# Kernel optimization log

Hardware: AMD Instinct MI355X
Metric: run time of the kernel (lower is better)

The kernel has to match this reference:

```python
import jax, jax.numpy as jnp
import numpy as np

B, T, D = 4, 4096, 1024
N, L = 2048, 768
H = 16
EPS = 1e-5

def layernorm(x, g, b):
    mu = jnp.mean(x, axis=-1, keepdims=True)
    var = jnp.mean((x - mu) ** 2, axis=-1, keepdims=True)
    return (x - mu) * jax.lax.rsqrt(var + EPS) * g + b

def setup_inputs() -> dict:
    key = jax.random.key(0)
    ks = jax.random.split(key, 8)
    s_d = 1.0 / np.sqrt(D)
    s_l = 1.0 / np.sqrt(L)
    return {
        "x1": jax.random.normal(ks[0], (B, T, D), jnp.float32),
        "x2": jax.random.normal(ks[1], (B, N, L), jnp.float32),
        "Wq": jax.random.normal(ks[2], (D, D), jnp.float32) * s_d,
        "bq": jnp.zeros((D,), jnp.float32),
        "Wk": jax.random.normal(ks[3], (L, D), jnp.float32) * s_l,
        "bk": jnp.zeros((D,), jnp.float32),
        "Wv": jax.random.normal(ks[4], (L, D), jnp.float32) * s_l,
        "bv": jnp.zeros((D,), jnp.float32),
        "Wh": jax.random.normal(ks[5], (D, D), jnp.float32) * s_d,
        "bh": jnp.zeros((D,), jnp.float32),
        "g1": jnp.ones((D,), jnp.float32),
        "b1": jnp.zeros((D,), jnp.float32),
        "g2": jnp.ones((L,), jnp.float32),
        "b2": jnp.zeros((L,), jnp.float32),
    }

def reference(x1, x2, Wq, bq, Wk, bk, Wv, bv, Wh, bh, g1, b1, g2, b2):
    nx1 = layernorm(x1, g1, b1)
    nx2 = layernorm(x2, g2, b2)
    q = (nx1 @ Wq + bq).reshape(B, T, H, D // H)
    k = (nx2 @ Wk + bk).reshape(B, N, H, D // H)
    v = (nx2 @ Wv + bv).reshape(B, N, H, D // H)
    q = jax.nn.softmax(q, axis=-1)
    k = jax.nn.softmax(k, axis=-1)
    # dropout p=0 -> identity
    attn = jnp.einsum('bnhd,bnhl->bhdl', k, v)          # [B,H,dh,dh]
    y = jnp.einsum('bthd,bhdl->bthl', q, attn).reshape(B, T, D)
    return x1 @ Wh + bh + y
```

## Files before the change

kernel.cpp:

```cpp
#include <hip/hip_runtime.h>


#define DEV __device__ __forceinline__

typedef unsigned short bf16_t;
typedef __attribute__((ext_vector_type(8))) __bf16 bf16x8;
typedef __attribute__((ext_vector_type(8))) unsigned short ushort8;
typedef __attribute__((ext_vector_type(4))) float f32x4;

DEV unsigned short f2bf(float f) {
  unsigned int u = __float_as_uint(f);
  unsigned int r = 0x7FFFu + ((u >> 16) & 1u);
  return (unsigned short)((u + r) >> 16);
}
DEV float bf2f(unsigned short u) { return __uint_as_float(((unsigned int)u) << 16); }

DEV void gld16(const void* g, void* l) {
  __builtin_amdgcn_global_load_lds((__attribute__((address_space(1))) void*)g,
                                   (__attribute__((address_space(3))) void*)l, 16, 0, 0);
}

__global__ __launch_bounds__(256) void wprep_kernel(
    const float* __restrict__ Wq, const float* __restrict__ Wk,
    const float* __restrict__ Wv, const float* __restrict__ Wh,
    bf16_t* __restrict__ Wqf, bf16_t* __restrict__ Wkf,
    bf16_t* __restrict__ Wvf, bf16_t* __restrict__ Whf) {
  int t = blockIdx.x;
  const float* src; bf16_t* dst; int KB;
  if (t < 1024)      { src = Wq; dst = Wqf; KB = 32; }
  else if (t < 1792) { src = Wk; dst = Wkf; KB = 24; t -= 1024; }
  else if (t < 2560) { src = Wv; dst = Wvf; KB = 24; t -= 1792; }
  else               { src = Wh; dst = Whf; KB = 32; t -= 2560; }
  int tk = t >> 5, tn = t & 31;
  __shared__ float tile[32][33];
  int tx = threadIdx.x & 31, ty = threadIdx.x >> 5;
#pragma unroll
  for (int i = 0; i < 4; ++i) {
    int r = ty + i * 8;
    tile[r][tx] = src[(size_t)(tk * 32 + r) * 1024 + tn * 32 + tx];
  }
  __syncthreads();
  int tid = threadIdx.x;
  if (tid < 128) {
    int rt = tid >> 6, p = (tid >> 4) & 3, ri = tid & 15;
    ushort8 v;
#pragma unroll
    for (int ko = 0; ko < 8; ++ko)
      v[ko] = f2bf(tile[p * 8 + ko][rt * 16 + ri]);
    size_t off = ((size_t)(tn * 2 + rt) * KB + tk) * 512 + p * 128 + ri * 8;
    *(ushort8*)&dst[off] = v;
  }
}

__global__ __launch_bounds__(256) void ln1_kernel(
    const float* __restrict__ x1, const float* __restrict__ g1, const float* __restrict__ b1,
    bf16_t* __restrict__ nx1f, bf16_t* __restrict__ x1f) {
  __shared__ bf16_t stash[16 * 1032];
  __shared__ float murs[16][2];
  int rt = blockIdx.x, tid = threadIdx.x;
  {
    int rowl = tid >> 4, ci = tid & 15;
    size_t base = ((size_t)rt * 16 + rowl) * 1024;
    float s = 0.f, s2 = 0.f;
#pragma unroll
    for (int j = 0; j < 16; ++j) {
      int k0 = ci * 4 + j * 64;
      float4 f = *(const float4*)&x1[base + k0];
      s += f.x + f.y + f.z + f.w;
      s2 += f.x * f.x + f.y * f.y + f.z * f.z + f.w * f.w;
      ushort4 u;
      u.x = f2bf(f.x); u.y = f2bf(f.y); u.z = f2bf(f.z); u.w = f2bf(f.w);
      *(ushort4*)&stash[rowl * 1032 + k0] = u;
    }
#pragma unroll
    for (int off = 1; off < 16; off <<= 1) {
      s  += __shfl_xor(s, off);
      s2 += __shfl_xor(s2, off);
    }
    if (ci == 0) {
      float mu = s * (1.0f / 1024.0f);
      float var = s2 * (1.0f / 1024.0f) - mu * mu;
      murs[rowl][0] = mu;
      murs[rowl][1] = rsqrtf(var + 1e-5f);
    }
  }
  __syncthreads();
  {
    int ri = tid & 15, pg = tid >> 4;
    float mu = murs[ri][0], rs = murs[ri][1];
#pragma unroll
    for (int t = 0; t < 8; ++t) {
      int P = pg * 8 + t;
      ushort8 raw = *(const ushort8*)&stash[ri * 1032 + P * 8];
      float4 ga = *(const float4*)&g1[P * 8], gb = *(const float4*)&g1[P * 8 + 4];
      float4 ba = *(const float4*)&b1[P * 8], bb = *(const float4*)&b1[P * 8 + 4];
      float gv[8] = {ga.x, ga.y, ga.z, ga.w, gb.x, gb.y, gb.z, gb.w};
      float bv[8] = {ba.x, ba.y, ba.z, ba.w, bb.x, bb.y, bb.z, bb.w};
      ushort8 nv;
#pragma unroll
      for (int ko = 0; ko < 8; ++ko)
        nv[ko] = f2bf((bf2f(raw[ko]) - mu) * rs * gv[ko] + bv[ko]);
      size_t off = ((size_t)rt * 32 + (P >> 2)) * 512 + (P & 3) * 128 + ri * 8;
      *(ushort8*)&nx1f[off] = nv;
      *(ushort8*)&x1f[off] = raw;
    }
  }
}

__global__ __launch_bounds__(256) void ln2_kernel(
    const float* __restrict__ x2, const float* __restrict__ g2, const float* __restrict__ b2,
    bf16_t* __restrict__ nx2f) {
  __shared__ bf16_t stash[16 * 776];
  __shared__ float murs[16][2];
  int rt = blockIdx.x, tid = threadIdx.x;
  {
    int rowl = tid >> 4, ci = tid & 15;
    size_t base = ((size_t)rt * 16 + rowl) * 768;
    float s = 0.f, s2 = 0.f;
#pragma unroll
    for (int j = 0; j < 12; ++j) {
      int k0 = ci * 4 + j * 64;
      float4 f = *(const float4*)&x2[base + k0];
      s += f.x + f.y + f.z + f.w;
      s2 += f.x * f.x + f.y * f.y + f.z * f.z + f.w * f.w;
      ushort4 u;
      u.x = f2bf(f.x); u.y = f2bf(f.y); u.z = f2bf(f.z); u.w = f2bf(f.w);
      *(ushort4*)&stash[rowl * 776 + k0] = u;
    }
#pragma unroll
    for (int off = 1; off < 16; off <<= 1) {
      s  += __shfl_xor(s, off);
      s2 += __shfl_xor(s2, off);
    }
    if (ci == 0) {
      float mu = s * (1.0f / 768.0f);
      float var = s2 * (1.0f / 768.0f) - mu * mu;
      murs[rowl][0] = mu;
      murs[rowl][1] = rsqrtf(var + 1e-5f);
    }
  }
  __syncthreads();
  {
    int ri = tid & 15, pg = tid >> 4;
    float mu = murs[ri][0], rs = murs[ri][1];
#pragma unroll
    for (int t = 0; t < 6; ++t) {
      int P = pg * 6 + t;
      ushort8 raw = *(const ushort8*)&stash[ri * 776 + P * 8];
      float4 ga = *(const float4*)&g2[P * 8], gb = *(const float4*)&g2[P * 8 + 4];
      float4 ba = *(const float4*)&b2[P * 8], bb = *(const float4*)&b2[P * 8 + 4];
      float gv[8] = {ga.x, ga.y, ga.z, ga.w, gb.x, gb.y, gb.z, gb.w};
      float bv[8] = {ba.x, ba.y, ba.z, ba.w, bb.x, bb.y, bb.z, bb.w};
      ushort8 nv;
#pragma unroll
      for (int ko = 0; ko < 8; ++ko)
        nv[ko] = f2bf((bf2f(raw[ko]) - mu) * rs * gv[ko] + bv[ko]);
      size_t off = ((size_t)rt * 24 + (P >> 2)) * 512 + (P & 3) * 128 + ri * 8;
      *(ushort8*)&nx2f[off] = nv;
    }
  }
}

__global__ __launch_bounds__(256, 2) void gemm_qkv_kernel(
    const bf16_t* __restrict__ nx1f, const bf16_t* __restrict__ Wqf,
    const float* __restrict__ bq, bf16_t* __restrict__ qout,
    const bf16_t* __restrict__ nx2f, const bf16_t* __restrict__ Wkf,
    const float* __restrict__ bk, bf16_t* __restrict__ kout,
    const bf16_t* __restrict__ Wvf, const float* __restrict__ bv,
    bf16_t* __restrict__ vout) {
  __shared__ bf16_t Bs[2 * 16 * 512];
  int id = blockIdx.x;
  const bf16_t *A, *BT; const float* bias; bf16_t* out;
  int nk, bm, bn, do_softmax;
  if (id < 512) {
    A = nx1f; BT = Wqf; bias = bq; out = qout; nk = 32;
    bm = id & 127; bn = id >> 7; do_softmax = 1;
  } else if (id < 768) {
    id -= 512; A = nx2f; BT = Wkf; bias = bk; out = kout; nk = 24;
    bm = id & 63; bn = id >> 6; do_softmax = 1;
  } else {
    id -= 768; A = nx2f; BT = Wvf; bias = bv; out = vout; nk = 24;
    bm = id & 63; bn = id >> 6; do_softmax = 0;
  }
  int tid = threadIdx.x, lane = tid & 63, wid = tid >> 6;
  int wm = wid & 1, wn = wid >> 1;

  const bf16_t* ap[4];
#pragma unroll
  for (int mi = 0; mi < 4; ++mi)
    ap[mi] = A + ((size_t)(bm * 8 + wm * 4 + mi) * nk) * 512 + lane * 8;
  const bf16_t* sp[4];
#pragma unroll
  for (int i = 0; i < 4; ++i)
    sp[i] = BT + ((size_t)(bn * 16 + wid * 4 + i) * nk) * 512 + lane * 8;

  f32x4 acc[4][8];
#pragma unroll
  for (int i = 0; i < 4; ++i)
#pragma unroll
    for (int j = 0; j < 8; ++j) acc[i][j] = {0.f, 0.f, 0.f, 0.f};

  bf16x8 acur[4], anxt[4];
#pragma unroll
  for (int i = 0; i < 4; ++i)
    gld16(sp[i], (void*)&Bs[(wid * 4 + i) * 512 + lane * 8]);
#pragma unroll
  for (int mi = 0; mi < 4; ++mi) acur[mi] = *(const bf16x8*)ap[mi];

  for (int kt = 0; kt < nk; ++kt) {
    int cb = kt & 1;
    if (kt + 1 < nk) {
      int nb = cb ^ 1;
#pragma unroll
      for (int i = 0; i < 4; ++i)
        gld16(sp[i] + (kt + 1) * 512, (void*)&Bs[nb * 8192 + (wid * 4 + i) * 512 + lane * 8]);
#pragma unroll
      for (int mi = 0; mi < 4; ++mi) anxt[mi] = *(const bf16x8*)(ap[mi] + (kt + 1) * 512);
      asm volatile("s_waitcnt vmcnt(8)\n\ts_barrier" ::: "memory");
    } else {
      asm volatile("s_waitcnt vmcnt(0)\n\ts_barrier" ::: "memory");
    }
    bf16x8 bfr[8];
#pragma unroll
    for (int ni = 0; ni < 8; ++ni)
      bfr[ni] = *(const bf16x8*)&Bs[cb * 8192 + (wn * 8 + ni) * 512 + lane * 8];
#pragma unroll
    for (int mi = 0; mi < 4; ++mi)
#pragma unroll
      for (int ni = 0; ni < 8; ++ni)
        acc[mi][ni] = __builtin_amdgcn_mfma_f32_16x16x32_bf16(acur[mi], bfr[ni], acc[mi][ni], 0, 0, 0);
    asm volatile("s_waitcnt lgkmcnt(0)\n\ts_barrier" ::: "memory");
#pragma unroll
    for (int mi = 0; mi < 4; ++mi) acur[mi] = anxt[mi];
  }

  int colg0 = bn * 256 + wn * 128;
  float bvv[8];
#pragma unroll
  for (int ni = 0; ni < 8; ++ni) bvv[ni] = bias[colg0 + ni * 16 + (lane & 15)];
#pragma unroll
  for (int mi = 0; mi < 4; ++mi) {
#pragma unroll
    for (int r = 0; r < 4; ++r) {
      int row = bm * 128 + wm * 64 + mi * 16 + (lane >> 4) * 4 + r;
      float vx[8];
#pragma unroll
      for (int ni = 0; ni < 8; ++ni) vx[ni] = acc[mi][ni][r] + bvv[ni];
      if (do_softmax) {
#pragma unroll
        for (int g = 0; g < 2; ++g) {
          float ssum = 0.f;
#pragma unroll
          for (int j = 0; j < 4; ++j) { vx[g * 4 + j] = __expf(vx[g * 4 + j]); ssum += vx[g * 4 + j]; }
#pragma unroll
          for (int off = 1; off < 16; off <<= 1) ssum += __shfl_xor(ssum, off);
          float inv = 1.0f / ssum;
#pragma unroll
          for (int j = 0; j < 4; ++j) vx[g * 4 + j] *= inv;
        }
      }
#pragma unroll
      for (int ni = 0; ni < 8; ++ni)
        out[(size_t)row * 1024 + colg0 + ni * 16 + (lane & 15)] = f2bf(vx[ni]);
    }
  }
}

__global__ __launch_bounds__(256) void attn_partial_kernel(
    const bf16_t* __restrict__ kq, const bf16_t* __restrict__ vq,
    float* __restrict__ part) {
  int bh = blockIdx.x >> 3, c = blockIdx.x & 7;
  int b = bh >> 4, h = bh & 15;
  int tid = threadIdx.x;
  int td = tid & 15, tl = tid >> 4;
  __shared__ float ks[32][64];
  __shared__ float vs[32][64];
  float acc[4][4];
#pragma unroll
  for (int i = 0; i < 4; ++i)
#pragma unroll
    for (int j = 0; j < 4; ++j) acc[i][j] = 0.f;
  for (int s = 0; s < 8; ++s) {
    __syncthreads();
    int nr = tid >> 3, col = (tid & 7) * 8;
    int n = c * 256 + s * 32 + nr;
    size_t goff = ((size_t)(b * 2048 + n)) * 1024 + h * 64 + col;
    ushort8 lk = *(const ushort8*)&kq[goff];
    ushort8 lv = *(const ushort8*)&vq[goff];
#pragma unroll
    for (int j = 0; j < 8; ++j) {
      ks[nr][col + j] = bf2f(lk[j]);
      vs[nr][col + j] = bf2f(lv[j]);
    }
    __syncthreads();
#pragma unroll
    for (int nn = 0; nn < 32; ++nn) {
      float4 kv = *(const float4*)&ks[nn][td * 4];
      float4 vv = *(const float4*)&vs[nn][tl * 4];
      float ka[4] = {kv.x, kv.y, kv.z, kv.w};
      float va[4] = {vv.x, vv.y, vv.z, vv.w};
#pragma unroll
      for (int i = 0; i < 4; ++i)
#pragma unroll
        for (int j = 0; j < 4; ++j) acc[i][j] += ka[i] * va[j];
    }
  }
#pragma unroll
  for (int i = 0; i < 4; ++i)
#pragma unroll
    for (int j = 0; j < 4; ++j) {
      int d = td * 4 + i, l = tl * 4 + j;
      part[(((size_t)bh * 8 + c) * 64 + d) * 64 + l] = acc[i][j];
    }
}

__global__ __launch_bounds__(256) void attn_finalize_kernel(
    const float* __restrict__ part, bf16_t* __restrict__ attnT) {
  int bh = blockIdx.x, tid = threadIdx.x;
  for (int t = tid; t < 4096; t += 256) {
    int d = t >> 6, l = t & 63;
    float s = 0.f;
#pragma unroll
    for (int c = 0; c < 8; ++c)
      s += part[(((size_t)bh * 8 + c) * 64 + d) * 64 + l];
    attnT[((size_t)bh * 64 + l) * 64 + d] = f2bf(s);
  }
}

__global__ __launch_bounds__(256, 2) void gemm_final_kernel(
    const bf16_t* __restrict__ x1f, const bf16_t* __restrict__ Whf,
    const float* __restrict__ bias, const bf16_t* __restrict__ qb,
    const bf16_t* __restrict__ attnT, float* __restrict__ out) {
  __shared__ bf16_t Bs[2 * 16 * 512];
  const int nk = 32;
  int tid = threadIdx.x;
  int bm = blockIdx.x, bn = blockIdx.y;
  int lane = tid & 63, wid = tid >> 6;
  int wm = wid & 1, wn = wid >> 1;
  int b = bm >> 5;
  int klane = (lane >> 4) * 8;

  const bf16_t* ap[4];
#pragma unroll
  for (int mi = 0; mi < 4; ++mi)
    ap[mi] = x1f + ((size_t)(bm * 8 + wm * 4 + mi) * nk) * 512 + lane * 8;
  const bf16_t* sp[4];
#pragma unroll
  for (int i = 0; i < 4; ++i)
    sp[i] = Whf + ((size_t)(bn * 16 + wid * 4 + i) * nk) * 512 + lane * 8;

  f32x4 acc[4][8];
#pragma unroll
  for (int i = 0; i < 4; ++i)
#pragma unroll
    for (int j = 0; j < 8; ++j) acc[i][j] = {0.f, 0.f, 0.f, 0.f};

  bf16x8 acur[4], anxt[4];
#pragma unroll
  for (int i = 0; i < 4; ++i)
    gld16(sp[i], (void*)&Bs[(wid * 4 + i) * 512 + lane * 8]);
#pragma unroll
  for (int mi = 0; mi < 4; ++mi) acur[mi] = *(const bf16x8*)ap[mi];

  for (int kt = 0; kt < nk; ++kt) {
    int cb = kt & 1;
    if (kt + 1 < nk) {
      int nb = cb ^ 1;
#pragma unroll
      for (int i = 0; i < 4; ++i)
        gld16(sp[i] + (kt + 1) * 512, (void*)&Bs[nb * 8192 + (wid * 4 + i) * 512 + lane * 8]);
#pragma unroll
      for (int mi = 0; mi < 4; ++mi) anxt[mi] = *(const bf16x8*)(ap[mi] + (kt + 1) * 512);
      asm volatile("s_waitcnt vmcnt(8)\n\ts_barrier" ::: "memory");
    } else {
      asm volatile("s_waitcnt vmcnt(0)\n\ts_barrier" ::: "memory");
    }
    bf16x8 bfr[8];
#pragma unroll
    for (int ni = 0; ni < 8; ++ni)
      bfr[ni] = *(const bf16x8*)&Bs[cb * 8192 + (wn * 8 + ni) * 512 + lane * 8];
#pragma unroll
    for (int mi = 0; mi < 4; ++mi)
#pragma unroll
      for (int ni = 0; ni < 8; ++ni)
        acc[mi][ni] = __builtin_amdgcn_mfma_f32_16x16x32_bf16(acur[mi], bfr[ni], acc[mi][ni], 0, 0, 0);
    asm volatile("s_waitcnt lgkmcnt(0)\n\ts_barrier" ::: "memory");
#pragma unroll
    for (int mi = 0; mi < 4; ++mi) acur[mi] = anxt[mi];
  }

  {
    int h0 = bn * 4 + wn * 2;
#pragma unroll
    for (int k2 = 0; k2 < 2; ++k2) {
      bf16x8 aq[2][4], bt[8];
#pragma unroll
      for (int g = 0; g < 2; ++g)
#pragma unroll
        for (int mi = 0; mi < 4; ++mi)
          aq[g][mi] = *(const bf16x8*)(qb
              + (size_t)(bm * 128 + wm * 64 + mi * 16 + (lane & 15)) * 1024
              + (h0 + g) * 64 + k2 * 32 + klane);
#pragma unroll
      for (int ni = 0; ni < 8; ++ni)
        bt[ni] = *(const bf16x8*)(attnT
            + ((size_t)(b * 16 + h0 + (ni >> 2)) * 64 + (ni & 3) * 16 + (lane & 15)) * 64
            + k2 * 32 + klane);
#pragma unroll
      for (int mi = 0; mi < 4; ++mi)
#pragma unroll
        for (int ni = 0; ni < 8; ++ni)
          acc[mi][ni] = __builtin_amdgcn_mfma_f32_16x16x32_bf16(aq[ni >> 2][mi], bt[ni], acc[mi][ni], 0, 0, 0);
    }
  }

  int colg0 = bn * 256 + wn * 128;
  float bvv[8];
#pragma unroll
  for (int ni = 0; ni < 8; ++ni) bvv[ni] = bias[colg0 + ni * 16 + (lane & 15)];
#pragma unroll
  for (int mi = 0; mi < 4; ++mi)
#pragma unroll
    for (int r = 0; r < 4; ++r) {
      int row = bm * 128 + wm * 64 + mi * 16 + (lane >> 4) * 4 + r;
#pragma unroll
      for (int ni = 0; ni < 8; ++ni)
        out[(size_t)row * 1024 + colg0 + ni * 16 + (lane & 15)] = acc[mi][ni][r] + bvv[ni];
    }
}

extern "C" void kernel_launch(void* const* d_in, const int* in_sizes, int n_in,
                              void* d_out, int out_size, void* d_ws, size_t ws_size,
                              hipStream_t stream) {
  const float* x1 = (const float*)d_in[0];
  const float* x2 = (const float*)d_in[1];
  const float* Wq = (const float*)d_in[2];
  const float* bq = (const float*)d_in[3];
  const float* Wk = (const float*)d_in[4];
  const float* bk = (const float*)d_in[5];
  const float* Wv = (const float*)d_in[6];
  const float* bv = (const float*)d_in[7];
  const float* Wh = (const float*)d_in[8];
  const float* bh = (const float*)d_in[9];
  const float* g1 = (const float*)d_in[10];
  const float* b1 = (const float*)d_in[11];
  const float* g2 = (const float*)d_in[12];
  const float* b2 = (const float*)d_in[13];
  float* out = (float*)d_out;

  char* w = (char*)d_ws;
  bf16_t* nx1f = (bf16_t*)w; w += (size_t)16384 * 1024 * 2;
  bf16_t* x1f  = (bf16_t*)w; w += (size_t)16384 * 1024 * 2;
  bf16_t* nx2f = (bf16_t*)w; w += (size_t)8192 * 768 * 2;
  bf16_t* Wqf  = (bf16_t*)w; w += (size_t)1024 * 1024 * 2;
  bf16_t* Wkf  = (bf16_t*)w; w += (size_t)1024 * 768 * 2;
  bf16_t* Wvf  = (bf16_t*)w; w += (size_t)1024 * 768 * 2;
  bf16_t* Whf  = (bf16_t*)w; w += (size_t)1024 * 1024 * 2;
  bf16_t* qb   = (bf16_t*)w; w += (size_t)16384 * 1024 * 2;
  bf16_t* kbuf = (bf16_t*)w; w += (size_t)8192 * 1024 * 2;
  bf16_t* vbuf = (bf16_t*)w; w += (size_t)8192 * 1024 * 2;
  float*  part = (float*)w;  w += (size_t)64 * 8 * 64 * 64 * 4;
  bf16_t* attnT = (bf16_t*)w; w += (size_t)64 * 64 * 64 * 2;

  wprep_kernel<<<dim3(3584), dim3(256), 0, stream>>>(Wq, Wk, Wv, Wh, Wqf, Wkf, Wvf, Whf);
  ln1_kernel<<<dim3(1024), dim3(256), 0, stream>>>(x1, g1, b1, nx1f, x1f);
  ln2_kernel<<<dim3(512), dim3(256), 0, stream>>>(x2, g2, b2, nx2f);
  gemm_qkv_kernel<<<dim3(1024), dim3(256), 0, stream>>>(
      nx1f, Wqf, bq, qb, nx2f, Wkf, bk, kbuf, Wvf, bv, vbuf);
  attn_partial_kernel<<<dim3(512), dim3(256), 0, stream>>>(kbuf, vbuf, part);
  attn_finalize_kernel<<<dim3(64), dim3(256), 0, stream>>>(part, attnT);
  gemm_final_kernel<<<dim3(128, 4), dim3(256), 0, stream>>>(x1f, Whf, bh, qb, attnT, out);
}
```

Baseline: 316.6 us.

## Deepen GEMM k-loop pipeline to triple buffering with prefetch distance two

Replaces the double-buffered K loop in the QKV and final GEMM kernels with a shared templated loop that keeps three LDS stages and three A-register sets. Loads run two k-steps ahead, with vmcnt waits adjusted to match, so more memory latency is hidden behind MFMA work. In exchange the LDS footprint grows from 32KB to 48KB per block and register pressure rises, which could lower occupancy at launch_bounds(256,2).

```diff
diff --git a/kernel.cpp b/kernel.cpp
--- a/kernel.cpp
+++ b/kernel.cpp
@@ -18,6 +18,65 @@
 DEV void gld16(const void* g, void* l) {
   __builtin_amdgcn_global_load_lds((__attribute__((address_space(1))) void*)g,
                                    (__attribute__((address_space(3))) void*)l, 16, 0, 0);
+}
+
+template <int NK>
+DEV void kloop3(const bf16_t* const ap[4], const bf16_t* const sp[4],
+                bf16_t* Bs, int lane, int wid, int wn, f32x4 acc[4][8]) {
+  bf16x8 a0[4], a1[4], a2[4];
+#pragma unroll
+  for (int i = 0; i < 4; ++i)
+    gld16(sp[i], (void*)&Bs[(wid * 4 + i) * 512 + lane * 8]);
+#pragma unroll
+  for (int mi = 0; mi < 4; ++mi) a0[mi] = *(const bf16x8*)ap[mi];
+#pragma unroll
+  for (int i = 0; i < 4; ++i)
+    gld16(sp[i] + 512, (void*)&Bs[8192 + (wid * 4 + i) * 512 + lane * 8]);
+#pragma unroll
+  for (int mi = 0; mi < 4; ++mi) a1[mi] = *(const bf16x8*)(ap[mi] + 512);
+
+#define KSTEP(ktv, PH, ACUR, AFILL, ISSUE, VMSTR)                                      \
+  do {                                                                                 \
+    if (ISSUE) {                                                                       \
+      _Pragma("unroll")                                                                \
+      for (int i = 0; i < 4; ++i)                                                      \
+        gld16(sp[i] + ((ktv) + 2) * 512,                                               \
+              (void*)&Bs[(((PH) + 2) % 3) * 8192 + (wid * 4 + i) * 512 + lane * 8]);   \
+      _Pragma("unroll")                                                                \
+      for (int mi = 0; mi < 4; ++mi)                                                   \
+        AFILL[mi] = *(const bf16x8*)(ap[mi] + ((ktv) + 2) * 512);                      \
+    }                                                                                  \
+    asm volatile("s_waitcnt " VMSTR "\n\ts_barrier" ::: "memory");                     \
+    bf16x8 bfr[8];                                                                     \
+    _Pragma("unroll")                                                                  \
+    for (int ni = 0; ni < 8; ++ni)                                                     \
+      bfr[ni] = *(const bf16x8*)&Bs[(PH) * 8192 + (wn * 8 + ni) * 512 + lane * 8];     \
+    _Pragma("unroll")                                                                  \
+    for (int mi = 0; mi < 4; ++mi)                                                     \
+      _Pragma("unroll")                                                                \
+      for (int ni = 0; ni < 8; ++ni)                                                   \
+        acc[mi][ni] =                                                                  \
+            __builtin_amdgcn_mfma_f32_16x16x32_bf16(ACUR[mi], bfr[ni], acc[mi][ni],    \
+                                                    0, 0, 0);                          \
+    asm volatile("s_waitcnt lgkmcnt(0)\n\ts_barrier" ::: "memory");                    \
+  } while (0)
+
+  constexpr int TFULL = (NK - (NK % 3 == 0 ? 3 : 2)) / 3;
+  for (int kb = 0; kb < TFULL; ++kb) {
+    int kt = kb * 3;
+    KSTEP(kt,     0, a0, a2, true, "vmcnt(16)");
+    KSTEP(kt + 1, 1, a1, a0, true, "vmcnt(16)");
+    KSTEP(kt + 2, 2, a2, a1, true, "vmcnt(16)");
+  }
+  if constexpr (NK % 3 == 0) {
+    KSTEP(NK - 3, 0, a0, a2, true,  "vmcnt(16)");
+    KSTEP(NK - 2, 1, a1, a0, false, "vmcnt(8)");
+    KSTEP(NK - 1, 2, a2, a1, false, "vmcnt(0)");
+  } else {
+    KSTEP(NK - 2, 0, a0, a2, false, "vmcnt(8)");
+    KSTEP(NK - 1, 1, a1, a0, false, "vmcnt(0)");
+  }
+#undef KSTEP
 }
 
 __global__ __launch_bounds__(256) void wprep_kernel(
@@ -168,7 +227,7 @@
     const float* __restrict__ bk, bf16_t* __restrict__ kout,
     const bf16_t* __restrict__ Wvf, const float* __restrict__ bv,
     bf16_t* __restrict__ vout) {
-  __shared__ bf16_t Bs[2 * 16 * 512];
+  __shared__ bf16_t Bs[3 * 16 * 512];
   int id = blockIdx.x;
   const bf16_t *A, *BT; const float* bias; bf16_t* out;
   int nk, bm, bn, do_softmax;
@@ -200,39 +259,8 @@
 #pragma unroll
     for (int j = 0; j < 8; ++j) acc[i][j] = {0.f, 0.f, 0.f, 0.f};
 
-  bf16x8 acur[4], anxt[4];
-#pragma unroll
-  for (int i = 0; i < 4; ++i)
-    gld16(sp[i], (void*)&Bs[(wid * 4 + i) * 512 + lane * 8]);
-#pragma unroll
-  for (int mi = 0; mi < 4; ++mi) acur[mi] = *(const bf16x8*)ap[mi];
-
-  for (int kt = 0; kt < nk; ++kt) {
-    int cb = kt & 1;
-    if (kt + 1 < nk) {
-      int nb = cb ^ 1;
-#pragma unroll
-      for (int i = 0; i < 4; ++i)
-        gld16(sp[i] + (kt + 1) * 512, (void*)&Bs[nb * 8192 + (wid * 4 + i) * 512 + lane * 8]);
-#pragma unroll
-      for (int mi = 0; mi < 4; ++mi) anxt[mi] = *(const bf16x8*)(ap[mi] + (kt + 1) * 512);
-      asm volatile("s_waitcnt vmcnt(8)\n\ts_barrier" ::: "memory");
-    } else {
-      asm volatile("s_waitcnt vmcnt(0)\n\ts_barrier" ::: "memory");
-    }
-    bf16x8 bfr[8];
-#pragma unroll
-    for (int ni = 0; ni < 8; ++ni)
-      bfr[ni] = *(const bf16x8*)&Bs[cb * 8192 + (wn * 8 + ni) * 512 + lane * 8];
-#pragma unroll
-    for (int mi = 0; mi < 4; ++mi)
-#pragma unroll
-      for (int ni = 0; ni < 8; ++ni)
-        acc[mi][ni] = __builtin_amdgcn_mfma_f32_16x16x32_bf16(acur[mi], bfr[ni], acc[mi][ni], 0, 0, 0);
-    asm volatile("s_waitcnt lgkmcnt(0)\n\ts_barrier" ::: "memory");
-#pragma unroll
-    for (int mi = 0; mi < 4; ++mi) acur[mi] = anxt[mi];
-  }
+  if (nk == 32) kloop3<32>(ap, sp, Bs, lane, wid, wn, acc);
+  else          kloop3<24>(ap, sp, Bs, lane, wid, wn, acc);
 
   int colg0 = bn * 256 + wn * 128;
   float bvv[8];
@@ -331,7 +359,7 @@
     const bf16_t* __restrict__ x1f, const bf16_t* __restrict__ Whf,
     const float* __restrict__ bias, const bf16_t* __restrict__ qb,
     const bf16_t* __restrict__ attnT, float* __restrict__ out) {
-  __shared__ bf16_t Bs[2 * 16 * 512];
+  __shared__ bf16_t Bs[3 * 16 * 512];
   const int nk = 32;
   int tid = threadIdx.x;
   int bm = blockIdx.x, bn = blockIdx.y;
@@ -355,39 +383,7 @@
 #pragma unroll
     for (int j = 0; j < 8; ++j) acc[i][j] = {0.f, 0.f, 0.f, 0.f};
 
-  bf16x8 acur[4], anxt[4];
-#pragma unroll
-  for (int i = 0; i < 4; ++i)
-    gld16(sp[i], (void*)&Bs[(wid * 4 + i) * 512 + lane * 8]);
-#pragma unroll
-  for (int mi = 0; mi < 4; ++mi) acur[mi] = *(const bf16x8*)ap[mi];
-
-  for (int kt = 0; kt < nk; ++kt) {
-    int cb = kt & 1;
-    if (kt + 1 < nk) {
-      int nb = cb ^ 1;
-#pragma unroll
-      for (int i = 0; i < 4; ++i)
-        gld16(sp[i] + (kt + 1) * 512, (void*)&Bs[nb * 8192 + (wid * 4 + i) * 512 + lane * 8]);
-#pragma unroll
-      for (int mi = 0; mi < 4; ++mi) anxt[mi] = *(const bf16x8*)(ap[mi] + (kt + 1) * 512);
-      asm volatile("s_waitcnt vmcnt(8)\n\ts_barrier" ::: "memory");
-    } else {
-      asm volatile("s_waitcnt vmcnt(0)\n\ts_barrier" ::: "memory");
-    }
-    bf16x8 bfr[8];
-#pragma unroll
-    for (int ni = 0; ni < 8; ++ni)
-      bfr[ni] = *(const bf16x8*)&Bs[cb * 8192 + (wn * 8 + ni) * 512 + lane * 8];
-#pragma unroll
-    for (int mi = 0; mi < 4; ++mi)
-#pragma unroll
-      for (int ni = 0; ni < 8; ++ni)
-        acc[mi][ni] = __builtin_amdgcn_mfma_f32_16x16x32_bf16(acur[mi], bfr[ni], acc[mi][ni], 0, 0, 0);
-    asm volatile("s_waitcnt lgkmcnt(0)\n\ts_barrier" ::: "memory");
-#pragma unroll
-    for (int mi = 0; mi < 4; ++mi) acur[mi] = anxt[mi];
-  }
+  kloop3<32>(ap, sp, Bs, lane, wid, wn, acc);
 
   {
     int h0 = bn * 4 + wn * 2;
```

Measured after the change: 431.6 us. +36.3%, slower.

## Deepen GEMM B-tile pipeline to four LDS stages and drop second barrier

Applied to the files above, without the earlier changes.

Both GEMM kernels now run a shared k-loop helper that keeps four LDS buffers for the weight tiles and prefetches two k-steps ahead instead of one. The second per-iteration barrier with its lgkmcnt wait is removed, relying on the four-deep ring to stop a buffer being overwritten while another wave still reads it. The aim is to hide more global-load latency and cut synchronisation per k-step. The cost is doubled LDS per block (64 KB), which may reduce occupancy below the two blocks per CU set by the launch bounds.

```diff
diff --git a/kernel.cpp b/kernel.cpp
--- a/kernel.cpp
+++ b/kernel.cpp
@@ -18,6 +18,70 @@
 DEV void gld16(const void* g, void* l) {
   __builtin_amdgcn_global_load_lds((__attribute__((address_space(1))) void*)g,
                                    (__attribute__((address_space(3))) void*)l, 16, 0, 0);
+}
+
+DEV void kloop(int nk, const bf16_t* const ap[4], const bf16_t* const sp[4],
+               bf16_t* Bs, int lane, int wid, int wn, f32x4 acc[4][8]) {
+  bf16x8 acur[4], anxt[4];
+#pragma unroll
+  for (int i = 0; i < 4; ++i)
+    gld16(sp[i], (void*)&Bs[(wid * 4 + i) * 512 + lane * 8]);
+#pragma unroll
+  for (int mi = 0; mi < 4; ++mi) acur[mi] = *(const bf16x8*)ap[mi];
+#pragma unroll
+  for (int i = 0; i < 4; ++i)
+    gld16(sp[i] + 512, (void*)&Bs[8192 + (wid * 4 + i) * 512 + lane * 8]);
+
+  for (int kt = 0; kt < nk - 2; ++kt) {
+#pragma unroll
+    for (int mi = 0; mi < 4; ++mi)
+      anxt[mi] = *(const bf16x8*)(ap[mi] + (kt + 1) * 512);
+#pragma unroll
+    for (int i = 0; i < 4; ++i)
+      gld16(sp[i] + (kt + 2) * 512,
+            (void*)&Bs[((kt + 2) & 3) * 8192 + (wid * 4 + i) * 512 + lane * 8]);
+    asm volatile("s_waitcnt vmcnt(12)\n\ts_barrier" ::: "memory");
+    bf16x8 bfr[8];
+#pragma unroll
+    for (int ni = 0; ni < 8; ++ni)
+      bfr[ni] = *(const bf16x8*)&Bs[(kt & 3) * 8192 + (wn * 8 + ni) * 512 + lane * 8];
+#pragma unroll
+    for (int mi = 0; mi < 4; ++mi)
+#pragma unroll
+      for (int ni = 0; ni < 8; ++ni)
+        acc[mi][ni] = __builtin_amdgcn_mfma_f32_16x16x32_bf16(acur[mi], bfr[ni], acc[mi][ni], 0, 0, 0);
+#pragma unroll
+    for (int mi = 0; mi < 4; ++mi) acur[mi] = anxt[mi];
+  }
+  {
+#pragma unroll
+    for (int mi = 0; mi < 4; ++mi)
+      anxt[mi] = *(const bf16x8*)(ap[mi] + (nk - 1) * 512);
+    asm volatile("s_waitcnt vmcnt(8)\n\ts_barrier" ::: "memory");
+    bf16x8 bfr[8];
+#pragma unroll
+    for (int ni = 0; ni < 8; ++ni)
+      bfr[ni] = *(const bf16x8*)&Bs[((nk - 2) & 3) * 8192 + (wn * 8 + ni) * 512 + lane * 8];
+#pragma unroll
+    for (int mi = 0; mi < 4; ++mi)
+#pragma unroll
+      for (int ni = 0; ni < 8; ++ni)
+        acc[mi][ni] = __builtin_amdgcn_mfma_f32_16x16x32_bf16(acur[mi], bfr[ni], acc[mi][ni], 0, 0, 0);
+#pragma unroll
+    for (int mi = 0; mi < 4; ++mi) acur[mi] = anxt[mi];
+  }
+  {
+    asm volatile("s_waitcnt vmcnt(0)\n\ts_barrier" ::: "memory");
+    bf16x8 bfr[8];
+#pragma unroll
+    for (int ni = 0; ni < 8; ++ni)
+      bfr[ni] = *(const bf16x8*)&Bs[((nk - 1) & 3) * 8192 + (wn * 8 + ni) * 512 + lane * 8];
+#pragma unroll
+    for (int mi = 0; mi < 4; ++mi)
+#pragma unroll
+      for (int ni = 0; ni < 8; ++ni)
+        acc[mi][ni] = __builtin_amdgcn_mfma_f32_16x16x32_bf16(acur[mi], bfr[ni], acc[mi][ni], 0, 0, 0);
+  }
 }
 
 __global__ __launch_bounds__(256) void wprep_kernel(
@@ -168,7 +232,7 @@
     const float* __restrict__ bk, bf16_t* __restrict__ kout,
     const bf16_t* __restrict__ Wvf, const float* __restrict__ bv,
     bf16_t* __restrict__ vout) {
-  __shared__ bf16_t Bs[2 * 16 * 512];
+  __shared__ bf16_t Bs[4 * 16 * 512];
   int id = blockIdx.x;
   const bf16_t *A, *BT; const float* bias; bf16_t* out;
   int nk, bm, bn, do_softmax;
@@ -200,39 +264,7 @@
 #pragma unroll
     for (int j = 0; j < 8; ++j) acc[i][j] = {0.f, 0.f, 0.f, 0.f};
 
-  bf16x8 acur[4], anxt[4];
-#pragma unroll
-  for (int i = 0; i < 4; ++i)
-    gld16(sp[i], (void*)&Bs[(wid * 4 + i) * 512 + lane * 8]);
-#pragma unroll
-  for (int mi = 0; mi < 4; ++mi) acur[mi] = *(const bf16x8*)ap[mi];
-
-  for (int kt = 0; kt < nk; ++kt) {
-    int cb = kt & 1;
-    if (kt + 1 < nk) {
-      int nb = cb ^ 1;
-#pragma unroll
-      for (int i = 0; i < 4; ++i)
-        gld16(sp[i] + (kt + 1) * 512, (void*)&Bs[nb * 8192 + (wid * 4 + i) * 512 + lane * 8]);
-#pragma unroll
-      for (int mi = 0; mi < 4; ++mi) anxt[mi] = *(const bf16x8*)(ap[mi] + (kt + 1) * 512);
-      asm volatile("s_waitcnt vmcnt(8)\n\ts_barrier" ::: "memory");
-    } else {
-      asm volatile("s_waitcnt vmcnt(0)\n\ts_barrier" ::: "memory");
-    }
-    bf16x8 bfr[8];
-#pragma unroll
-    for (int ni = 0; ni < 8; ++ni)
-      bfr[ni] = *(const bf16x8*)&Bs[cb * 8192 + (wn * 8 + ni) * 512 + lane * 8];
-#pragma unroll
-    for (int mi = 0; mi < 4; ++mi)
-#pragma unroll
-      for (int ni = 0; ni < 8; ++ni)
-        acc[mi][ni] = __builtin_amdgcn_mfma_f32_16x16x32_bf16(acur[mi], bfr[ni], acc[mi][ni], 0, 0, 0);
-    asm volatile("s_waitcnt lgkmcnt(0)\n\ts_barrier" ::: "memory");
-#pragma unroll
-    for (int mi = 0; mi < 4; ++mi) acur[mi] = anxt[mi];
-  }
+  kloop(nk, ap, sp, Bs, lane, wid, wn, acc);
 
   int colg0 = bn * 256 + wn * 128;
   float bvv[8];
@@ -331,7 +363,7 @@
     const bf16_t* __restrict__ x1f, const bf16_t* __restrict__ Whf,
     const float* __restrict__ bias, const bf16_t* __restrict__ qb,
     const bf16_t* __restrict__ attnT, float* __restrict__ out) {
-  __shared__ bf16_t Bs[2 * 16 * 512];
+  __shared__ bf16_t Bs[4 * 16 * 512];
   const int nk = 32;
   int tid = threadIdx.x;
   int bm = blockIdx.x, bn = blockIdx.y;
@@ -355,39 +387,7 @@
 #pragma unroll
     for (int j = 0; j < 8; ++j) acc[i][j] = {0.f, 0.f, 0.f, 0.f};
 
-  bf16x8 acur[4], anxt[4];
-#pragma unroll
-  for (int i = 0; i < 4; ++i)
-    gld16(sp[i], (void*)&Bs[(wid * 4 + i) * 512 + lane * 8]);
-#pragma unroll
-  for (int mi = 0; mi < 4; ++mi) acur[mi] = *(const bf16x8*)ap[mi];
-
-  for (int kt = 0; kt < nk; ++kt) {
-    int cb = kt & 1;
-    if (kt + 1 < nk) {
-      int nb = cb ^ 1;
-#pragma unroll
-      for (int i = 0; i < 4; ++i)
-        gld16(sp[i] + (kt + 1) * 512, (void*)&Bs[nb * 8192 + (wid * 4 + i) * 512 + lane * 8]);
-#pragma unroll
-      for (int mi = 0; mi < 4; ++mi) anxt[mi] = *(const bf16x8*)(ap[mi] + (kt + 1) * 512);
-      asm volatile("s_waitcnt vmcnt(8)\n\ts_barrier" ::: "memory");
-    } else {
-      asm volatile("s_waitcnt vmcnt(0)\n\ts_barrier" ::: "memory");
-    }
-    bf16x8 bfr[8];
-#pragma unroll
-    for (int ni = 0; ni < 8; ++ni)
-      bfr[ni] = *(const bf16x8*)&Bs[cb * 8192 + (wn * 8 + ni) * 512 + lane * 8];
-#pragma unroll
-    for (int mi = 0; mi < 4; ++mi)
-#pragma unroll
-      for (int ni = 0; ni < 8; ++ni)
-        acc[mi][ni] = __builtin_amdgcn_mfma_f32_16x16x32_bf16(acur[mi], bfr[ni], acc[mi][ni], 0, 0, 0);
-    asm volatile("s_waitcnt lgkmcnt(0)\n\ts_barrier" ::: "memory");
-#pragma unroll
-    for (int mi = 0; mi < 4; ++mi) acur[mi] = anxt[mi];
-  }
+  kloop(nk, ap, sp, Bs, lane, wid, wn, acc);
 
   {
     int h0 = bn * 4 + wn * 2;
```

After: 318.3 us. Within noise of the previous version (+0.5%).

## Merge weight-prep and layernorm kernels; use MFMA for K^T V partials

Applied to the files above, without the earlier changes.

Folds the three preprocessing kernels (weight transpose/convert, LN1, LN2) into a single launch that dispatches on block index, sharing one LDS buffer. This removes two launch gaps and lets the small kernels run concurrently. It also rewrites the per-head K^T V partial reduction to stage K and V transposed in bf16 LDS and use 16x16x32 bf16 MFMA instead of scalar FP32 FMAs. The shared LDS is sized for the largest branch, which may lower occupancy for the weight blocks.

```diff
diff --git a/kernel.cpp b/kernel.cpp
--- a/kernel.cpp
+++ b/kernel.cpp
@@ -20,143 +20,149 @@
                                    (__attribute__((address_space(3))) void*)l, 16, 0, 0);
 }
 
-__global__ __launch_bounds__(256) void wprep_kernel(
+__global__ __launch_bounds__(256) void prep_kernel(
     const float* __restrict__ Wq, const float* __restrict__ Wk,
     const float* __restrict__ Wv, const float* __restrict__ Wh,
     bf16_t* __restrict__ Wqf, bf16_t* __restrict__ Wkf,
-    bf16_t* __restrict__ Wvf, bf16_t* __restrict__ Whf) {
-  int t = blockIdx.x;
-  const float* src; bf16_t* dst; int KB;
-  if (t < 1024)      { src = Wq; dst = Wqf; KB = 32; }
-  else if (t < 1792) { src = Wk; dst = Wkf; KB = 24; t -= 1024; }
-  else if (t < 2560) { src = Wv; dst = Wvf; KB = 24; t -= 1792; }
-  else               { src = Wh; dst = Whf; KB = 32; t -= 2560; }
-  int tk = t >> 5, tn = t & 31;
-  __shared__ float tile[32][33];
-  int tx = threadIdx.x & 31, ty = threadIdx.x >> 5;
-#pragma unroll
-  for (int i = 0; i < 4; ++i) {
-    int r = ty + i * 8;
-    tile[r][tx] = src[(size_t)(tk * 32 + r) * 1024 + tn * 32 + tx];
-  }
-  __syncthreads();
-  int tid = threadIdx.x;
-  if (tid < 128) {
-    int rt = tid >> 6, p = (tid >> 4) & 3, ri = tid & 15;
-    ushort8 v;
-#pragma unroll
-    for (int ko = 0; ko < 8; ++ko)
-      v[ko] = f2bf(tile[p * 8 + ko][rt * 16 + ri]);
-    size_t off = ((size_t)(tn * 2 + rt) * KB + tk) * 512 + p * 128 + ri * 8;
-    *(ushort8*)&dst[off] = v;
-  }
-}
-
-__global__ __launch_bounds__(256) void ln1_kernel(
-    const float* __restrict__ x1, const float* __restrict__ g1, const float* __restrict__ b1,
-    bf16_t* __restrict__ nx1f, bf16_t* __restrict__ x1f) {
-  __shared__ bf16_t stash[16 * 1032];
+    bf16_t* __restrict__ Wvf, bf16_t* __restrict__ Whf,
+    const float* __restrict__ x1, const float* __restrict__ g1,
+    const float* __restrict__ b1, bf16_t* __restrict__ nx1f,
+    bf16_t* __restrict__ x1f,
+    const float* __restrict__ x2, const float* __restrict__ g2,
+    const float* __restrict__ b2, bf16_t* __restrict__ nx2f) {
+  __shared__ __align__(16) char smem[16 * 1032 * 2];
   __shared__ float murs[16][2];
-  int rt = blockIdx.x, tid = threadIdx.x;
+  int blk = blockIdx.x, tid = threadIdx.x;
+
+  if (blk < 3584) {
+    int t = blk;
+    const float* src; bf16_t* dst; int KB;
+    if (t < 1024)      { src = Wq; dst = Wqf; KB = 32; }
+    else if (t < 1792) { src = Wk; dst = Wkf; KB = 24; t -= 1024; }
+    else if (t < 2560) { src = Wv; dst = Wvf; KB = 24; t -= 1792; }
+    else               { src = Wh; dst = Whf; KB = 32; t -= 2560; }
+    int tk = t >> 5, tn = t & 31;
+    float (*tile)[33] = (float(*)[33])smem;
+    int tx = tid & 31, ty = tid >> 5;
+#pragma unroll
+    for (int i = 0; i < 4; ++i) {
+      int r = ty + i * 8;
+      tile[r][tx] = src[(size_t)(tk * 32 + r) * 1024 + tn * 32 + tx];
+    }
+    __syncthreads();
+    if (tid < 128) {
+      int rt = tid >> 6, p = (tid >> 4) & 3, ri = tid & 15;
+      ushort8 v;
+#pragma unroll
+      for (int ko = 0; ko < 8; ++ko)
+        v[ko] = f2bf(tile[p * 8 + ko][rt * 16 + ri]);
+      size_t off = ((size_t)(tn * 2 + rt) * KB + tk) * 512 + p * 128 + ri * 8;
+      *(ushort8*)&dst[off] = v;
+    }
+    return;
+  }
+
+  if (blk < 4608) {
+    bf16_t* stash = (bf16_t*)smem;
+    int rt = blk - 3584;
+    {
+      int rowl = tid >> 4, ci = tid & 15;
+      size_t base = ((size_t)rt * 16 + rowl) * 1024;
+      float s = 0.f, s2 = 0.f;
+#pragma unroll
+      for (int j = 0; j < 16; ++j) {
+        int k0 = ci * 4 + j * 64;
+        float4 f = *(const float4*)&x1[base + k0];
+        s += f.x + f.y + f.z + f.w;
+        s2 += f.x * f.x + f.y * f.y + f.z * f.z + f.w * f.w;
+        ushort4 u;
+        u.x = f2bf(f.x); u.y = f2bf(f.y); u.z = f2bf(f.z); u.w = f2bf(f.w);
+        *(ushort4*)&stash[rowl * 1032 + k0] = u;
+      }
+#pragma unroll
+      for (int off = 1; off < 16; off <<= 1) {
+        s  += __shfl_xor(s, off);
+        s2 += __shfl_xor(s2, off);
+      }
+      if (ci == 0) {
+        float mu = s * (1.0f / 1024.0f);
+        float var = s2 * (1.0f / 1024.0f) - mu * mu;
+        murs[rowl][0] = mu;
+        murs[rowl][1] = rsqrtf(var + 1e-5f);
+      }
+    }
+    __syncthreads();
+    {
+      int ri = tid & 15, pg = tid >> 4;
+      float mu = murs[ri][0], rs = murs[ri][1];
+#pragma unroll
+      for (int t = 0; t < 8; ++t) {
+        int P = pg * 8 + t;
+        ushort8 raw = *(const ushort8*)&stash[ri * 1032 + P * 8];
+        float4 ga = *(const float4*)&g1[P * 8], gb = *(const float4*)&g1[P * 8 + 4];
+        float4 ba = *(const float4*)&b1[P * 8], bb = *(const float4*)&b1[P * 8 + 4];
+        float gv[8] = {ga.x, ga.y, ga.z, ga.w, gb.x, gb.y, gb.z, gb.w};
+        float bv[8] = {ba.x, ba.y, ba.z, ba.w, bb.x, bb.y, bb.z, bb.w};
+        ushort8 nv;
+#pragma unroll
+        for (int ko = 0; ko < 8; ++ko)
+          nv[ko] = f2bf((bf2f(raw[ko]) - mu) * rs * gv[ko] + bv[ko]);
+        size_t off = ((size_t)rt * 32 + (P >> 2)) * 512 + (P & 3) * 128 + ri * 8;
+        *(ushort8*)&nx1f[off] = nv;
+        *(ushort8*)&x1f[off] = raw;
+      }
+    }
+    return;
+  }
+
   {
-    int rowl = tid >> 4, ci = tid & 15;
-    size_t base = ((size_t)rt * 16 + rowl) * 1024;
-    float s = 0.f, s2 = 0.f;
-#pragma unroll
-    for (int j = 0; j < 16; ++j) {
-      int k0 = ci * 4 + j * 64;
-      float4 f = *(const float4*)&x1[base + k0];
-      s += f.x + f.y + f.z + f.w;
-      s2 += f.x * f.x + f.y * f.y + f.z * f.z + f.w * f.w;
-      ushort4 u;
-      u.x = f2bf(f.x); u.y = f2bf(f.y); u.z = f2bf(f.z); u.w = f2bf(f.w);
-      *(ushort4*)&stash[rowl * 1032 + k0] = u;
-    }
-#pragma unroll
-    for (int off = 1; off < 16; off <<= 1) {
-      s  += __shfl_xor(s, off);
-      s2 += __shfl_xor(s2, off);
-    }
-    if (ci == 0) {
-      float mu = s * (1.0f / 1024.0f);
-      float var = s2 * (1.0f / 1024.0f) - mu * mu;
-      murs[rowl][0] = mu;
-      murs[rowl][1] = rsqrtf(var + 1e-5f);
-    }
-  }
-  __syncthreads();
-  {
-    int ri = tid & 15, pg = tid >> 4;
-    float mu = murs[ri][0], rs = murs[ri][1];
-#pragma unroll
-    for (int t = 0; t < 8; ++t) {
-      int P = pg * 8 + t;
-      ushort8 raw = *(const ushort8*)&stash[ri * 1032 + P * 8];
-      float4 ga = *(const float4*)&g1[P * 8], gb = *(const float4*)&g1[P * 8 + 4];
-      float4 ba = *(const float4*)&b1[P * 8], bb = *(const float4*)&b1[P * 8 + 4];
-      float gv[8] = {ga.x, ga.y, ga.z, ga.w, gb.x, gb.y, gb.z, gb.w};
-      float bv[8] = {ba.x, ba.y, ba.z, ba.w, bb.x, bb.y, bb.z, bb.w};
-      ushort8 nv;
-#pragma unroll
-      for (int ko = 0; ko < 8; ++ko)
-        nv[ko] = f2bf((bf2f(raw[ko]) - mu) * rs * gv[ko] + bv[ko]);
-      size_t off = ((size_t)rt * 32 + (P >> 2)) * 512 + (P & 3) * 128 + ri * 8;
-      *(ushort8*)&nx1f[off] = nv;
-      *(ushort8*)&x1f[off] = raw;
-    }
-  }
-}
-
-__global__ __launch_bounds__(256) void ln2_kernel(
-    const float* __restrict__ x2, const float* __restrict__ g2, const float* __restrict__ b2,
-    bf16_t* __restrict__ nx2f) {
-  __shared__ bf16_t stash[16 * 776];
-  __shared__ float murs[16][2];
-  int rt = blockIdx.x, tid = threadIdx.x;
-  {
-    int rowl = tid >> 4, ci = tid & 15;
-    size_t base = ((size_t)rt * 16 + rowl) * 768;
-    float s = 0.f, s2 = 0.f;
-#pragma unroll
-    for (int j = 0; j < 12; ++j) {
-      int k0 = ci * 4 + j * 64;
-      float4 f = *(const float4*)&x2[base + k0];
-      s += f.x + f.y + f.z + f.w;
-      s2 += f.x * f.x + f.y * f.y + f.z * f.z + f.w * f.w;
-      ushort4 u;
-      u.x = f2bf(f.x); u.y = f2bf(f.y); u.z = f2bf(f.z); u.w = f2bf(f.w);
-      *(ushort4*)&stash[rowl * 776 + k0] = u;
-    }
-#pragma unroll
-    for (int off = 1; off < 16; off <<= 1) {
-      s  += __shfl_xor(s, off);
-      s2 += __shfl_xor(s2, off);
-    }
-    if (ci == 0) {
-      float mu = s * (1.0f / 768.0f);
-      float var = s2 * (1.0f / 768.0f) - mu * mu;
-      murs[rowl][0] = mu;
-      murs[rowl][1] = rsqrtf(var + 1e-5f);
-    }
-  }
-  __syncthreads();
-  {
-    int ri = tid & 15, pg = tid >> 4;
-    float mu = murs[ri][0], rs = murs[ri][1];
-#pragma unroll
-    for (int t = 0; t < 6; ++t) {
-      int P = pg * 6 + t;
-      ushort8 raw = *(const ushort8*)&stash[ri * 776 + P * 8];
-      float4 ga = *(const float4*)&g2[P * 8], gb = *(const float4*)&g2[P * 8 + 4];
-      float4 ba = *(const float4*)&b2[P * 8], bb = *(const float4*)&b2[P * 8 + 4];
-      float gv[8] = {ga.x, ga.y, ga.z, ga.w, gb.x, gb.y, gb.z, gb.w};
-      float bv[8] = {ba.x, ba.y, ba.z, ba.w, bb.x, bb.y, bb.z, bb.w};
-      ushort8 nv;
-#pragma unroll
-      for (int ko = 0; ko < 8; ++ko)
-        nv[ko] = f2bf((bf2f(raw[ko]) - mu) * rs * gv[ko] + bv[ko]);
-      size_t off = ((size_t)rt * 24 + (P >> 2)) * 512 + (P & 3) * 128 + ri * 8;
-      *(ushort8*)&nx2f[off] = nv;
+    bf16_t* stash = (bf16_t*)smem;
+    int rt = blk - 4608;
+    {
+      int rowl = tid >> 4, ci = tid & 15;
+      size_t base = ((size_t)rt * 16 + rowl) * 768;
+      float s = 0.f, s2 = 0.f;
+#pragma unroll
+      for (int j = 0; j < 12; ++j) {
+        int k0 = ci * 4 + j * 64;
+        float4 f = *(const float4*)&x2[base + k0];
+        s += f.x + f.y + f.z + f.w;
+        s2 += f.x * f.x + f.y * f.y + f.z * f.z + f.w * f.w;
+        ushort4 u;
+        u.x = f2bf(f.x); u.y = f2bf(f.y); u.z = f2bf(f.z); u.w = f2bf(f.w);
+        *(ushort4*)&stash[rowl * 776 + k0] = u;
+      }
+#pragma unroll
+      for (int off = 1; off < 16; off <<= 1) {
+        s  += __shfl_xor(s, off);
+        s2 += __shfl_xor(s2, off);
+      }
+      if (ci == 0) {
+        float mu = s * (1.0f / 768.0f);
+        float var = s2 * (1.0f / 768.0f) - mu * mu;
+        murs[rowl][0] = mu;
+        murs[rowl][1] = rsqrtf(var + 1e-5f);
+      }
+    }
+    __syncthreads();
+    {
+      int ri = tid & 15, pg = tid >> 4;
+      float mu = murs[ri][0], rs = murs[ri][1];
+#pragma unroll
+      for (int t = 0; t < 6; ++t) {
+        int P = pg * 6 + t;
+        ushort8 raw = *(const ushort8*)&stash[ri * 776 + P * 8];
+        float4 ga = *(const float4*)&g2[P * 8], gb = *(const float4*)&g2[P * 8 + 4];
+        float4 ba = *(const float4*)&b2[P * 8], bb = *(const float4*)&b2[P * 8 + 4];
+        float gv[8] = {ga.x, ga.y, ga.z, ga.w, gb.x, gb.y, gb.z, gb.w};
+        float bv[8] = {ba.x, ba.y, ba.z, ba.w, bb.x, bb.y, bb.z, bb.w};
+        ushort8 nv;
+#pragma unroll
+        for (int ko = 0; ko < 8; ++ko)
+          nv[ko] = f2bf((bf2f(raw[ko]) - mu) * rs * gv[ko] + bv[ko]);
+        size_t off = ((size_t)rt * 24 + (P >> 2)) * 512 + (P & 3) * 128 + ri * 8;
+        *(ushort8*)&nx2f[off] = nv;
+      }
     }
   }
 }
@@ -271,46 +277,41 @@
     float* __restrict__ part) {
   int bh = blockIdx.x >> 3, c = blockIdx.x & 7;
   int b = bh >> 4, h = bh & 15;
-  int tid = threadIdx.x;
-  int td = tid & 15, tl = tid >> 4;
-  __shared__ float ks[32][64];
-  __shared__ float vs[32][64];
-  float acc[4][4];
-#pragma unroll
-  for (int i = 0; i < 4; ++i)
-#pragma unroll
-    for (int j = 0; j < 4; ++j) acc[i][j] = 0.f;
+  int tid = threadIdx.x, lane = tid & 63, wid = tid >> 6;
+  __shared__ bf16_t Kt[64][40];
+  __shared__ bf16_t Vt[64][40];
+  f32x4 acc[4];
+#pragma unroll
+  for (int ni = 0; ni < 4; ++ni) acc[ni] = {0.f, 0.f, 0.f, 0.f};
+  int nl = tid & 31, d0 = (tid >> 5) * 8;
+  int m = lane & 15, kp = lane >> 4;
+
   for (int s = 0; s < 8; ++s) {
-    __syncthreads();
-    int nr = tid >> 3, col = (tid & 7) * 8;
-    int n = c * 256 + s * 32 + nr;
-    size_t goff = ((size_t)(b * 2048 + n)) * 1024 + h * 64 + col;
+    int n = c * 256 + s * 32 + nl;
+    size_t goff = ((size_t)(b * 2048 + n)) * 1024 + h * 64 + d0;
     ushort8 lk = *(const ushort8*)&kq[goff];
     ushort8 lv = *(const ushort8*)&vq[goff];
+    __syncthreads();
 #pragma unroll
     for (int j = 0; j < 8; ++j) {
-      ks[nr][col + j] = bf2f(lk[j]);
-      vs[nr][col + j] = bf2f(lv[j]);
+      Kt[d0 + j][nl] = lk[j];
+      Vt[d0 + j][nl] = lv[j];
     }
     __syncthreads();
-#pragma unroll
-    for (int nn = 0; nn < 32; ++nn) {
-      float4 kv = *(const float4*)&ks[nn][td * 4];
-      float4 vv = *(const float4*)&vs[nn][tl * 4];
-      float ka[4] = {kv.x, kv.y, kv.z, kv.w};
-      float va[4] = {vv.x, vv.y, vv.z, vv.w};
-#pragma unroll
-      for (int i = 0; i < 4; ++i)
-#pragma unroll
-        for (int j = 0; j < 4; ++j) acc[i][j] += ka[i] * va[j];
-    }
-  }
-#pragma unroll
-  for (int i = 0; i < 4; ++i)
-#pragma unroll
-    for (int j = 0; j < 4; ++j) {
-      int d = td * 4 + i, l = tl * 4 + j;
-      part[(((size_t)bh * 8 + c) * 64 + d) * 64 + l] = acc[i][j];
+    bf16x8 af = *(const bf16x8*)&Kt[wid * 16 + m][kp * 8];
+#pragma unroll
+    for (int ni = 0; ni < 4; ++ni) {
+      bf16x8 bf = *(const bf16x8*)&Vt[ni * 16 + m][kp * 8];
+      acc[ni] = __builtin_amdgcn_mfma_f32_16x16x32_bf16(af, bf, acc[ni], 0, 0, 0);
+    }
+  }
+#pragma unroll
+  for (int ni = 0; ni < 4; ++ni)
+#pragma unroll
+    for (int r = 0; r < 4; ++r) {
+      int d = wid * 16 + kp * 4 + r;
+      int l = ni * 16 + m;
+      part[(((size_t)bh * 8 + c) * 64 + d) * 64 + l] = acc[ni][r];
     }
 }
 
@@ -462,9 +463,9 @@
   float*  part = (float*)w;  w += (size_t)64 * 8 * 64 * 64 * 4;
   bf16_t* attnT = (bf16_t*)w; w += (size_t)64 * 64 * 64 * 2;
 
-  wprep_kernel<<<dim3(3584), dim3(256), 0, stream>>>(Wq, Wk, Wv, Wh, Wqf, Wkf, Wvf, Whf);
-  ln1_kernel<<<dim3(1024), dim3(256), 0, stream>>>(x1, g1, b1, nx1f, x1f);
-  ln2_kernel<<<dim3(512), dim3(256), 0, stream>>>(x2, g2, b2, nx2f);
+  prep_kernel<<<dim3(5120), dim3(256), 0, stream>>>(
+      Wq, Wk, Wv, Wh, Wqf, Wkf, Wvf, Whf,
+      x1, g1, b1, nx1f, x1f, x2, g2, b2, nx2f);
   gemm_qkv_kernel<<<dim3(1024), dim3(256), 0, stream>>>(
       nx1f, Wqf, bq, qb, nx2f, Wkf, bk, kbuf, Wvf, bv, vbuf);
   attn_partial_kernel<<<dim3(512), dim3(256), 0, stream>>>(kbuf, vbuf, part);
```

Result: faster. 299.3 us (-5.5%).
